# Kernel optimization log

Measured on AMD Instinct MI355X. Metric: run time of the kernel, lower is better.

Reference implementation:

```python
import jax, jax.numpy as jnp
import numpy as np

HEADS = 12
EPS_RMS = 1e-6
EPS_LN = 1e-5


def _rms_inorm(x, w):
    # torch.std over spatial dims (unbiased, ddof=1); no mean subtraction
    std = jnp.std(x, axis=(2, 3), keepdims=True, ddof=1)
    return x / (std + EPS_RMS) * w[None, :, None, None]


def _layernorm(x, w, b):
    m = jnp.mean(x, axis=-1, keepdims=True)
    v = jnp.var(x, axis=-1, keepdims=True)
    return (x - m) / jnp.sqrt(v + EPS_LN) * w + b


def setup_inputs() -> dict:
    key = jax.random.key(0)
    ks = jax.random.split(key, 16)
    B, C, H, W = 8, 768, 64, 64
    hd = C // HEADS
    s = 0.02
    return {
        "x": jax.random.normal(ks[0], (B, C, H, W), jnp.float32),
        "bcs": jnp.zeros((1, 2), jnp.int32),
        "norm1_w": jnp.ones((C,), jnp.float32),
        "norm2_w": jnp.ones((C,), jnp.float32),
        "mlpn_w": jnp.ones((C,), jnp.float32),
        "Win": jax.random.normal(ks[1], (3 * C, C), jnp.float32) * s,
        "bin_": jnp.zeros((3 * C,), jnp.float32),
        "Wout": jax.random.normal(ks[2], (C, C), jnp.float32) * s,
        "bout": jnp.zeros((C,), jnp.float32),
        "qn_w": jnp.ones((hd,), jnp.float32),
        "qn_b": jnp.zeros((hd,), jnp.float32),
        "kn_w": jnp.ones((hd,), jnp.float32),
        "kn_b": jnp.zeros((hd,), jnp.float32),
        "gamma_att": jnp.full((C,), 1e-6, jnp.float32),
        "gamma_mlp": jnp.full((C,), 1e-6, jnp.float32),
        "W1": jax.random.normal(ks[3], (C, 4 * C), jnp.float32) * s,
        "b1": jnp.zeros((4 * C,), jnp.float32),
        "W2": jax.random.normal(ks[4], (4 * C, C), jnp.float32) * s,
        "b2": jnp.zeros((C,), jnp.float32),
    }


def reference(x, bcs, norm1_w, norm2_w, mlpn_w, Win, bin_, Wout, bout,
              qn_w, qn_b, kn_w, kn_b, gamma_att, gamma_mlp, W1, b1, W2, b2):
    B, C, H, W = x.shape
    hd = C // HEADS
    scale = 1.0 / jnp.sqrt(jnp.asarray(hd, x.dtype))

    h = _rms_inorm(x, norm1_w)
    # 1x1 conv QKV: [B, 3C, H, W]
    qkv = jnp.einsum('bchw,oc->bohw', h, Win) + bin_[None, :, None, None]
    # b (he c3) h w -> b he h w c3, then split into q,k,v of head_dim each
    qkv = qkv.reshape(B, HEADS, 3 * hd, H, W).transpose(0, 1, 3, 4, 2)
    q, k, v = jnp.split(qkv, 3, axis=-1)  # each [B, he, H, W, hd]
    q = _layernorm(q, qn_w, qn_b)
    k = _layernorm(k, kn_w, kn_b)

    # row attention: attend along W for each row h
    sx = jnp.einsum('bnhqc,bnhkc->bnhqk', q, k) * scale
    xx = jnp.einsum('bnhqk,bnhkc->bnhqc', jax.nn.softmax(sx, axis=-1), v)
    # column attention: attend along H for each column w
    sy = jnp.einsum('bnqwc,bnkwc->bnwqk', q, k) * scale
    xy = jnp.einsum('bnwqk,bnkwc->bnqwc', jax.nn.softmax(sy, axis=-1), v)

    a = (xx + xy) * 0.5  # [B, he, H, W, hd]
    a = a.transpose(0, 1, 4, 2, 3).reshape(B, C, H, W)
    a = _rms_inorm(a, norm2_w)
    a = jnp.einsum('bchw,oc->bohw', a, Wout) + bout[None, :, None, None]
    x1 = a * gamma_att[None, :, None, None] + x

    t = x1.transpose(0, 2, 3, 1)  # [B, H, W, C]
    m = jax.nn.gelu(t @ W1 + b1, approximate=False) @ W2 + b2
    m = m.transpose(0, 3, 1, 2)
    m = _rms_inorm(m, mlpn_w)
    return x1 + gamma_mlp[None, :, None, None] * m
```

## Files before the change

kernel.cpp:

```cpp
#include <hip/hip_runtime.h>

typedef __attribute__((ext_vector_type(8))) short short8;
typedef __attribute__((ext_vector_type(4))) float f32x4;
typedef __attribute__((ext_vector_type(4))) unsigned short u16x4;
typedef __attribute__((ext_vector_type(8))) unsigned short u16x8;

#define BDIM 8
#define CDIM 768
#define C3 2304
#define C4 3072
#define HEADS 12
#define HD 64
#define HWD 4096
#define TOKS 32768

__device__ __forceinline__ float bf2f(unsigned short u) {
    union { unsigned int i; float f; } x; x.i = ((unsigned int)u) << 16; return x.f;
}
__device__ __forceinline__ unsigned short f2bf(float f) {
    union { float f; unsigned int i; } x; x.f = f;
    unsigned int r = x.i + 0x7FFFu + ((x.i >> 16) & 1u);
    return (unsigned short)(r >> 16);
}

__device__ __forceinline__ void gload_lds16(const unsigned short* g, unsigned short* l) {
    __builtin_amdgcn_global_load_lds(
        (const __attribute__((address_space(1))) void*)g,
        (__attribute__((address_space(3))) void*)l, 16, 0, 0);
}

__global__ __launch_bounds__(256) void convert_f32_bf16(
    const float* __restrict__ src, unsigned short* __restrict__ dst, int n)
{
    int i = (blockIdx.x * 256 + threadIdx.x) * 4;
    if (i + 3 >= n + 4) return;
    if (i + 3 < n) {
        float4 v = *(const float4*)&src[i];
        dst[i + 0] = f2bf(v.x); dst[i + 1] = f2bf(v.y);
        dst[i + 2] = f2bf(v.z); dst[i + 3] = f2bf(v.w);
    }
}

__global__ __launch_bounds__(256) void transpose_w(
    const float* __restrict__ src, unsigned short* __restrict__ dst, int R, int Cc)
{
    const int n0 = blockIdx.x * 64, k0 = blockIdx.y * 64;
    __shared__ float t[64][65];
    #pragma unroll
    for (int s = 0; s < 16; ++s) {
        int flat = threadIdx.x + 256 * s;
        int i = flat >> 6, j = flat & 63;
        t[i][j] = src[(long)(k0 + i) * Cc + n0 + j];
    }
    __syncthreads();
    #pragma unroll
    for (int s = 0; s < 16; ++s) {
        int flat = threadIdx.x + 256 * s;
        int jn = flat >> 6, ik = flat & 63;
        dst[(long)(n0 + jn) * R + k0 + ik] = f2bf(t[ik][jn]);
    }
}

__global__ __launch_bounds__(256) void stats_spatial_f32(
    const float* __restrict__ x, const float* __restrict__ wgt,
    float* __restrict__ sout, float eps)
{
    const int bc = blockIdx.x;
    const int c = bc % CDIM;
    const float4* p4 = (const float4*)(x + (long)bc * HWD);
    float s = 0.f, ss = 0.f;
    #pragma unroll
    for (int k = 0; k < 4; ++k) {
        float4 v = p4[threadIdx.x + 256 * k];
        s  += v.x + v.y + v.z + v.w;
        ss += v.x * v.x + v.y * v.y + v.z * v.z + v.w * v.w;
    }
    #pragma unroll
    for (int m = 1; m < 64; m <<= 1) { s += __shfl_xor(s, m); ss += __shfl_xor(ss, m); }
    __shared__ float rs[4], rss[4];
    int w = threadIdx.x >> 6, lane = threadIdx.x & 63;
    if (lane == 0) { rs[w] = s; rss[w] = ss; }
    __syncthreads();
    if (threadIdx.x == 0) {
        float S = rs[0] + rs[1] + rs[2] + rs[3];
        float Q = rss[0] + rss[1] + rss[2] + rss[3];
        float var = (Q - S * S * (1.f / 4096.f)) * (1.f / 4095.f);
        sout[bc] = wgt[c] / (sqrtf(var) + eps);
    }
}

__global__ __launch_bounds__(256) void stats_spatial_bf16(
    const unsigned short* __restrict__ t, const float* __restrict__ wgt,
    float* __restrict__ sout, float eps)
{
    const int b = blockIdx.x / 12, cg = blockIdx.x % 12;
    const int sub = threadIdx.x & 15, tr = threadIdx.x >> 4;
    const unsigned short* base = t + (long)b * HWD * CDIM + cg * 64 + sub * 4;
    float s[4] = {0.f, 0.f, 0.f, 0.f}, q[4] = {0.f, 0.f, 0.f, 0.f};
    for (int i = 0; i < 256; ++i) {
        const int token = tr + 16 * i;
        u16x4 v = *(const u16x4*)(base + (long)token * CDIM);
        #pragma unroll
        for (int j = 0; j < 4; ++j) { float f = bf2f(v[j]); s[j] += f; q[j] += f * f; }
    }
    __shared__ float ssum[16][64], ssq[16][64];
    #pragma unroll
    for (int j = 0; j < 4; ++j) { ssum[tr][sub * 4 + j] = s[j]; ssq[tr][sub * 4 + j] = q[j]; }
    __syncthreads();
    if (threadIdx.x < 64) {
        const int c = threadIdx.x;
        float S = 0.f, Q = 0.f;
        #pragma unroll
        for (int r = 0; r < 16; ++r) { S += ssum[r][c]; Q += ssq[r][c]; }
        const float var = (Q - S * S * (1.f / 4096.f)) * (1.f / 4095.f);
        const int cglob = cg * 64 + c;
        sout[b * CDIM + cglob] = wgt[cglob] / (sqrtf(var) + eps);
    }
}

__global__ __launch_bounds__(256) void make_h(
    const float* __restrict__ x, const float* __restrict__ s1,
    unsigned short* __restrict__ h)
{
    const int hw0 = blockIdx.x * 64, c0 = blockIdx.y * 64, b = blockIdx.z;
    __shared__ float t[64][65];
    #pragma unroll
    for (int s = 0; s < 16; ++s) {
        int flat = threadIdx.x + 256 * s;
        int ci = flat >> 6, hj = flat & 63;
        t[ci][hj] = x[(long)(b * CDIM + c0 + ci) * HWD + hw0 + hj];
    }
    __syncthreads();
    #pragma unroll
    for (int s = 0; s < 16; ++s) {
        int flat = threadIdx.x + 256 * s;
        int hi = flat >> 6, cj = flat & 63;
        float v = t[cj][hi] * s1[b * CDIM + c0 + cj];
        h[(long)(b * HWD + hw0 + hi) * CDIM + c0 + cj] = f2bf(v);
    }
}

template<int GELU>
__global__ __launch_bounds__(512, 4) void gemm256(
    const unsigned short* __restrict__ A, const unsigned short* __restrict__ BT,
    const float* __restrict__ bias, unsigned short* __restrict__ out,
    int M, int N, int K)
{
    extern __shared__ unsigned short smem[];
    const int tid = threadIdx.x;
    const int lane = tid & 63, w = tid >> 6;
    const int wm = w >> 1, wn = w & 1;
    const int lr = lane & 15, g = lane >> 4;

    const int nwg = gridDim.x;
    const int logical = (blockIdx.x & 7) * (nwg >> 3) + (blockIdx.x >> 3);
    const int gnx = N >> 7;
    const int n0 = (logical % gnx) << 7;
    const int m0 = (logical / gnx) << 8;

    const int ka = (((tid & 3) ^ ((tid >> 3) & 3)) << 3);
    const unsigned short* aS0 = A + (long)(m0 + (tid >> 2)) * K + ka;
    const unsigned short* aS1 = A + (long)(m0 + 128 + (tid >> 2)) * K + ka;
    const unsigned short* bS = BT + (long)(n0 + (tid >> 2)) * K + ka;
    unsigned short* dA0 = smem + (tid & ~63) * 8;
    unsigned short* dA1 = dA0 + 4096;
    unsigned short* dB  = smem + 16384 + (tid & ~63) * 8;

#define GSTAGE(S) do { \
        gload_lds16(aS0, dA0 + (S) * 8192); \
        gload_lds16(aS1, dA1 + (S) * 8192); \
        gload_lds16(bS,  dB  + (S) * 4096); \
        aS0 += 32; aS1 += 32; bS += 32; } while (0)

    const int nsub = K >> 5;
    const int koff = ((g ^ ((lr >> 1) & 3)) << 3);
    const unsigned short* baseA = smem + (wm * 64 + lr) * 32 + koff;
    const unsigned short* baseB = smem + 16384 + (wn * 64 + lr) * 32 + koff;

    f32x4 acc[4][4] = {};

    GSTAGE(0); GSTAGE(1);

#define SUBTILE(U, STG, WAITN) do { \
        asm volatile("s_waitcnt vmcnt(" #WAITN ")" ::: "memory"); \
        __builtin_amdgcn_s_barrier(); \
        short8 bf[4], af[4]; \
        _Pragma("unroll") \
        for (int ni = 0; ni < 4; ++ni) bf[ni] = *(const short8*)(baseB + (U) * 4096 + ni * 512); \
        _Pragma("unroll") \
        for (int mi = 0; mi < 4; ++mi) af[mi] = *(const short8*)(baseA + (U) * 8192 + mi * 512); \
        asm volatile("s_waitcnt lgkmcnt(0)" ::: "memory"); \
        __builtin_amdgcn_s_barrier(); \
        __builtin_amdgcn_sched_barrier(0); \
        STG; \
        __builtin_amdgcn_s_setprio(1); \
        _Pragma("unroll") \
        for (int mi = 0; mi < 4; ++mi) \
            _Pragma("unroll") \
            for (int ni = 0; ni < 4; ++ni) \
                acc[mi][ni] = __builtin_amdgcn_mfma_f32_16x16x32_bf16(af[mi], bf[ni], acc[mi][ni], 0, 0, 0); \
        __builtin_amdgcn_s_setprio(0); \
        __builtin_amdgcn_sched_barrier(0); } while (0)

    for (int j2 = 0; j2 + 2 < nsub; j2 += 2) {
        SUBTILE(0, GSTAGE(0), 3);
        SUBTILE(1, GSTAGE(1), 3);
    }
    SUBTILE(0, , 3);
    SUBTILE(1, , 0);
#undef SUBTILE
#undef GSTAGE

    #pragma unroll
    for (int mi = 0; mi < 4; ++mi) {
        #pragma unroll
        for (int ni = 0; ni < 4; ++ni) {
            const int gcol = n0 + wn * 64 + ni * 16 + lr;
            const float bv = bias[gcol];
            #pragma unroll
            for (int r = 0; r < 4; ++r) {
                const int grow = m0 + wm * 64 + mi * 16 + g * 4 + r;
                float v = acc[mi][ni][r] + bv;
                if (GELU) v = 0.5f * v * (1.f + erff(v * 0.70710678118f));
                out[(long)grow * N + gcol] = f2bf(v);
            }
        }
    }
}

__global__ __launch_bounds__(256) void qk_layernorm(
    unsigned short* __restrict__ qkv,
    const float* __restrict__ qw, const float* __restrict__ qb,
    const float* __restrict__ kw, const float* __restrict__ kb)
{
    const int pairIdx = blockIdx.x * 16 + (threadIdx.x >> 4);
    const int token = pairIdx / HEADS, he = pairIdx % HEADS;
    const int c4 = (threadIdx.x & 15) * 4;
    const long base = (long)token * C3 + he * 192;
    #pragma unroll
    for (int which = 0; which < 2; ++which) {
        const long off = base + which * 64 + c4;
        u16x4 v = *(u16x4*)&qkv[off];
        float f[4];
        #pragma unroll
        for (int j = 0; j < 4; ++j) f[j] = bf2f(v[j]);
        float s = f[0] + f[1] + f[2] + f[3];
        float q = f[0] * f[0] + f[1] * f[1] + f[2] * f[2] + f[3] * f[3];
        #pragma unroll
        for (int m = 1; m < 16; m <<= 1) { s += __shfl_xor(s, m); q += __shfl_xor(q, m); }
        const float mean = s * (1.f / 64.f);
        const float var = q * (1.f / 64.f) - mean * mean;
        const float rstd = rsqrtf(var + 1e-5f);
        const float* W = which ? kw : qw;
        const float* Bv = which ? kb : qb;
        u16x4 o;
        #pragma unroll
        for (int j = 0; j < 4; ++j)
            o[j] = f2bf((f[j] - mean) * rstd * W[c4 + j] + Bv[c4 + j]);
        *(u16x4*)&qkv[off] = o;
    }
}

template<int AXIS>
__global__ __launch_bounds__(128) void attn_axial(
    const unsigned short* __restrict__ qkv, unsigned short* __restrict__ a)
{
    __shared__ unsigned short lds[2][2][64 * 72];
    const int tid = threadIdx.x;
    const int lane = tid & 63, w = tid >> 6;
    const int lineG = blockIdx.x * 2 + w;
    const int b = lineG / 768;
    const int rem = lineG - b * 768;
    const int he = rem >> 6, line = rem & 63;
    const int ts = (AXIS == 0) ? 1 : 64;
    const long token0 = (long)b * HWD + (AXIS == 0 ? line * 64 : line);
    const long qbase = token0 * C3 + he * 192;
    unsigned short* VT = &lds[w][0][0];
    unsigned short* P  = &lds[w][1][0];
    const int lr = lane & 15, g = lane >> 4;

    {
        const int keyr = lane >> 3, d8 = (lane & 7) << 3;
        #pragma unroll
        for (int it = 0; it < 8; ++it) {
            const int key = it * 8 + keyr;
            u16x8 v = *(const u16x8*)&qkv[qbase + (long)key * ts * C3 + 128 + d8];
            #pragma unroll
            for (int j = 0; j < 8; ++j) VT[(d8 + j) * 72 + key] = v[j];
        }
    }

    short8 qf[4][2], kf[4][2];
    #pragma unroll
    for (int i = 0; i < 4; ++i)
        #pragma unroll
        for (int kk = 0; kk < 2; ++kk) {
            const long rb = qbase + (long)(i * 16 + lr) * ts * C3 + kk * 32 + g * 8;
            qf[i][kk] = *(const short8*)&qkv[rb];
            kf[i][kk] = *(const short8*)&qkv[rb + 64];
        }

    f32x4 acc[4][4] = {};
    #pragma unroll
    for (int mi = 0; mi < 4; ++mi)
        #pragma unroll
        for (int ni = 0; ni < 4; ++ni) {
            acc[mi][ni] = __builtin_amdgcn_mfma_f32_16x16x32_bf16(qf[mi][0], kf[ni][0], acc[mi][ni], 0, 0, 0);
            acc[mi][ni] = __builtin_amdgcn_mfma_f32_16x16x32_bf16(qf[mi][1], kf[ni][1], acc[mi][ni], 0, 0, 0);
        }

    #pragma unroll
    for (int mi = 0; mi < 4; ++mi)
        #pragma unroll
        for (int r = 0; r < 4; ++r) {
            float mx = -1e30f;
            #pragma unroll
            for (int ni = 0; ni < 4; ++ni) {
                float v = acc[mi][ni][r] * 0.125f; acc[mi][ni][r] = v; mx = fmaxf(mx, v);
            }
            #pragma unroll
            for (int m = 1; m < 16; m <<= 1) mx = fmaxf(mx, __shfl_xor(mx, m));
            float s = 0.f;
            #pragma unroll
            for (int ni = 0; ni < 4; ++ni) {
                float e = __expf(acc[mi][ni][r] - mx); acc[mi][ni][r] = e; s += e;
            }
            #pragma unroll
            for (int m = 1; m < 16; m <<= 1) s += __shfl_xor(s, m);
            const float inv = 1.f / s;
            const int row = mi * 16 + 4 * g + r;
            #pragma unroll
            for (int ni = 0; ni < 4; ++ni)
                P[row * 72 + ni * 16 + lr] = f2bf(acc[mi][ni][r] * inv);
        }
    __syncthreads();

    short8 pa[4][2], vb[4][2];
    #pragma unroll
    for (int i = 0; i < 4; ++i)
        #pragma unroll
        for (int kk = 0; kk < 2; ++kk) {
            pa[i][kk] = *(const short8*)&P[(i * 16 + lr) * 72 + kk * 32 + g * 8];
            vb[i][kk] = *(const short8*)&VT[(i * 16 + lr) * 72 + kk * 32 + g * 8];
        }
    f32x4 o2[4][4] = {};
    #pragma unroll
    for (int mi = 0; mi < 4; ++mi)
        #pragma unroll
        for (int ni = 0; ni < 4; ++ni) {
            o2[mi][ni] = __builtin_amdgcn_mfma_f32_16x16x32_bf16(pa[mi][0], vb[ni][0], o2[mi][ni], 0, 0, 0);
            o2[mi][ni] = __builtin_amdgcn_mfma_f32_16x16x32_bf16(pa[mi][1], vb[ni][1], o2[mi][ni], 0, 0, 0);
        }

    #pragma unroll
    for (int mi = 0; mi < 4; ++mi)
        #pragma unroll
        for (int r = 0; r < 4; ++r) {
            const int q = mi * 16 + 4 * g + r;
            const long tok = token0 + (long)q * ts;
            #pragma unroll
            for (int ni = 0; ni < 4; ++ni) {
                const int d = ni * 16 + lr;
                const long addr = tok * CDIM + he * 64 + d;
                const float v = o2[mi][ni][r] * 0.5f;
                if (AXIS == 0) a[addr] = f2bf(v);
                else           a[addr] = f2bf(bf2f(a[addr]) + v);
            }
        }
}

__global__ __launch_bounds__(256) void scale_inplace(
    unsigned short* __restrict__ a, const float* __restrict__ s2)
{
    const long i = ((long)blockIdx.x * 256 + threadIdx.x) * 4;
    const int c = (int)(i % CDIM);
    const int b = (int)(i / ((long)CDIM * HWD));
    u16x4 v = *(u16x4*)&a[i];
    u16x4 o;
    #pragma unroll
    for (int j = 0; j < 4; ++j) o[j] = f2bf(bf2f(v[j]) * s2[b * CDIM + c + j]);
    *(u16x4*)&a[i] = o;
}

__global__ __launch_bounds__(256) void x1_combine(
    const unsigned short* __restrict__ o, const float* __restrict__ x,
    const float* __restrict__ gamma, float* __restrict__ dout,
    unsigned short* __restrict__ x1b)
{
    const int hw0 = blockIdx.x * 64, c0 = blockIdx.y * 64, b = blockIdx.z;
    __shared__ float t[64][65];
    #pragma unroll
    for (int s = 0; s < 16; ++s) {
        int flat = threadIdx.x + 256 * s;
        int i = flat >> 6, j = flat & 63;
        t[i][j] = bf2f(o[(long)(b * HWD + hw0 + i) * CDIM + c0 + j]);
    }
    __syncthreads();
    #pragma unroll
    for (int s = 0; s < 16; ++s) {
        int flat = threadIdx.x + 256 * s;
        int j = flat >> 6, i = flat & 63;
        const long xi = (long)(b * CDIM + c0 + j) * HWD + hw0 + i;
        float v = x[xi] + gamma[c0 + j] * t[i][j];
        dout[xi] = v;
        t[i][j] = v;
    }
    __syncthreads();
    #pragma unroll
    for (int s = 0; s < 16; ++s) {
        int flat = threadIdx.x + 256 * s;
        int i = flat >> 6, j = flat & 63;
        x1b[(long)(b * HWD + hw0 + i) * CDIM + c0 + j] = f2bf(t[i][j]);
    }
}

__global__ __launch_bounds__(256) void final_combine(
    const unsigned short* __restrict__ m, const float* __restrict__ gm,
    const float* __restrict__ s3, float* __restrict__ dout)
{
    const int hw0 = blockIdx.x * 64, c0 = blockIdx.y * 64, b = blockIdx.z;
    __shared__ float t[64][65];
    #pragma unroll
    for (int s = 0; s < 16; ++s) {
        int flat = threadIdx.x + 256 * s;
        int i = flat >> 6, j = flat & 63;
        t[i][j] = bf2f(m[(long)(b * HWD + hw0 + i) * CDIM + c0 + j]);
    }
    __syncthreads();
    #pragma unroll
    for (int s = 0; s < 16; ++s) {
        int flat = threadIdx.x + 256 * s;
        int j = flat >> 6, i = flat & 63;
        const long xi = (long)(b * CDIM + c0 + j) * HWD + hw0 + i;
        dout[xi] = dout[xi] + gm[c0 + j] * s3[b * CDIM + c0 + j] * t[i][j];
    }
}

extern "C" void kernel_launch(void* const* d_in, const int* in_sizes, int n_in,
                              void* d_out, int out_size, void* d_ws, size_t ws_size,
                              hipStream_t stream) {
    const float* x      = (const float*)d_in[0];
    const float* n1w    = (const float*)d_in[2];
    const float* n2w    = (const float*)d_in[3];
    const float* mlw    = (const float*)d_in[4];
    const float* Win    = (const float*)d_in[5];
    const float* bin    = (const float*)d_in[6];
    const float* Wout   = (const float*)d_in[7];
    const float* bout   = (const float*)d_in[8];
    const float* qn_w   = (const float*)d_in[9];
    const float* qn_b   = (const float*)d_in[10];
    const float* kn_w   = (const float*)d_in[11];
    const float* kn_b   = (const float*)d_in[12];
    const float* gatt   = (const float*)d_in[13];
    const float* gmlp   = (const float*)d_in[14];
    const float* W1     = (const float*)d_in[15];
    const float* b1     = (const float*)d_in[16];
    const float* W2     = (const float*)d_in[17];
    const float* b2     = (const float*)d_in[18];
    float* dout = (float*)d_out;
    char* ws = (char*)d_ws;

    unsigned short* wQ  = (unsigned short*)(ws);
    unsigned short* wO  = (unsigned short*)(ws + (4L << 20));
    unsigned short* w1t = (unsigned short*)(ws + (6L << 20));
    unsigned short* w2t = (unsigned short*)(ws + (11L << 20));
    float* s1 = (float*)(ws + (16L << 20));
    float* s2 = s1 + 6144;
    float* s3 = s2 + 6144;
    unsigned short* bufH = (unsigned short*)(ws + (17L << 20));
    unsigned short* bufQ = (unsigned short*)(ws + (65L << 20));
    unsigned short* bufA = (unsigned short*)(ws + (209L << 20));

    convert_f32_bf16<<<1728, 256, 0, stream>>>(Win, wQ, C3 * CDIM);
    convert_f32_bf16<<<576, 256, 0, stream>>>(Wout, wO, CDIM * CDIM);
    transpose_w<<<dim3(C4 / 64, CDIM / 64), 256, 0, stream>>>(W1, w1t, CDIM, C4);
    transpose_w<<<dim3(CDIM / 64, C4 / 64), 256, 0, stream>>>(W2, w2t, C4, CDIM);

    stats_spatial_f32<<<BDIM * CDIM, 256, 0, stream>>>(x, n1w, s1, 1e-6f);
    make_h<<<dim3(64, 12, 8), 256, 0, stream>>>(x, s1, bufH);

    gemm256<0><<<(TOKS / 256) * (C3 / 128), 512, 49152, stream>>>(bufH, wQ, bin, bufQ, TOKS, C3, CDIM);
    qk_layernorm<<<TOKS * HEADS / 16, 256, 0, stream>>>(bufQ, qn_w, qn_b, kn_w, kn_b);

    attn_axial<0><<<BDIM * HEADS * 64 / 2, 128, 0, stream>>>(bufQ, bufA);
    attn_axial<1><<<BDIM * HEADS * 64 / 2, 128, 0, stream>>>(bufQ, bufA);

    stats_spatial_bf16<<<BDIM * 12, 256, 0, stream>>>(bufA, n2w, s2, 1e-6f);
    scale_inplace<<<TOKS * CDIM / 1024, 256, 0, stream>>>(bufA, s2);
    gemm256<0><<<(TOKS / 256) * (CDIM / 128), 512, 49152, stream>>>(bufA, wO, bout, bufH, TOKS, CDIM, CDIM);
    x1_combine<<<dim3(64, 12, 8), 256, 0, stream>>>(bufH, x, gatt, dout, bufA);

    for (int ch = 0; ch < 2; ++ch) {
        const unsigned short* x1c = bufA + (long)ch * 16384 * CDIM;
        unsigned short* mc = bufH + (long)ch * 16384 * CDIM;
        gemm256<1><<<(16384 / 256) * (C4 / 128), 512, 49152, stream>>>(x1c, w1t, b1, bufQ, 16384, C4, CDIM);
        gemm256<0><<<(16384 / 256) * (CDIM / 128), 512, 49152, stream>>>(bufQ, w2t, b2, mc, 16384, CDIM, C4);
    }

    stats_spatial_bf16<<<BDIM * 12, 256, 0, stream>>>(bufH, mlw, s3, 1e-6f);
    final_combine<<<dim3(64, 12, 8), 256, 0, stream>>>(bufH, gmlp, s3, dout);
}
```

Measured before the change: 923.1 us.

## Fuse QK layernorm into axial attention and drop fp32 x1 round-trip

Removes the standalone qk_layernorm pass. Each axial attention kernel now normalizes its Q and K fragments in registers as it loads them, using cross-lane shuffles, so the in-place read and write of the Q/K part of the qkv buffer goes away. The cost is doing the layernorm twice, once per axis. Separately, x1_combine no longer writes fp32 x1 into the output. final_combine rebuilds the result from the bf16 x1 copy plus the scaled MLP branch, which cuts fp32 traffic but adds bf16 rounding to the residual term.

```diff
diff --git a/kernel.cpp b/kernel.cpp
--- a/kernel.cpp
+++ b/kernel.cpp
@@ -228,42 +228,12 @@
     }
 }
 
-__global__ __launch_bounds__(256) void qk_layernorm(
-    unsigned short* __restrict__ qkv,
-    const float* __restrict__ qw, const float* __restrict__ qb,
-    const float* __restrict__ kw, const float* __restrict__ kb)
-{
-    const int pairIdx = blockIdx.x * 16 + (threadIdx.x >> 4);
-    const int token = pairIdx / HEADS, he = pairIdx % HEADS;
-    const int c4 = (threadIdx.x & 15) * 4;
-    const long base = (long)token * C3 + he * 192;
-    #pragma unroll
-    for (int which = 0; which < 2; ++which) {
-        const long off = base + which * 64 + c4;
-        u16x4 v = *(u16x4*)&qkv[off];
-        float f[4];
-        #pragma unroll
-        for (int j = 0; j < 4; ++j) f[j] = bf2f(v[j]);
-        float s = f[0] + f[1] + f[2] + f[3];
-        float q = f[0] * f[0] + f[1] * f[1] + f[2] * f[2] + f[3] * f[3];
-        #pragma unroll
-        for (int m = 1; m < 16; m <<= 1) { s += __shfl_xor(s, m); q += __shfl_xor(q, m); }
-        const float mean = s * (1.f / 64.f);
-        const float var = q * (1.f / 64.f) - mean * mean;
-        const float rstd = rsqrtf(var + 1e-5f);
-        const float* W = which ? kw : qw;
-        const float* Bv = which ? kb : qb;
-        u16x4 o;
-        #pragma unroll
-        for (int j = 0; j < 4; ++j)
-            o[j] = f2bf((f[j] - mean) * rstd * W[c4 + j] + Bv[c4 + j]);
-        *(u16x4*)&qkv[off] = o;
-    }
-}
-
 template<int AXIS>
 __global__ __launch_bounds__(128) void attn_axial(
-    const unsigned short* __restrict__ qkv, unsigned short* __restrict__ a)
+    const unsigned short* __restrict__ qkv,
+    const float* __restrict__ qn_w, const float* __restrict__ qn_b,
+    const float* __restrict__ kn_w, const float* __restrict__ kn_b,
+    unsigned short* __restrict__ a)
 {
     __shared__ unsigned short lds[2][2][64 * 72];
     const int tid = threadIdx.x;
@@ -292,13 +262,40 @@
 
     short8 qf[4][2], kf[4][2];
     #pragma unroll
-    for (int i = 0; i < 4; ++i)
-        #pragma unroll
-        for (int kk = 0; kk < 2; ++kk) {
-            const long rb = qbase + (long)(i * 16 + lr) * ts * C3 + kk * 32 + g * 8;
-            qf[i][kk] = *(const short8*)&qkv[rb];
-            kf[i][kk] = *(const short8*)&qkv[rb + 64];
-        }
+    for (int i = 0; i < 4; ++i) {
+        const long rb = qbase + (long)(i * 16 + lr) * ts * C3 + g * 8;
+        u16x8 qv0 = *(const u16x8*)&qkv[rb];
+        u16x8 qv1 = *(const u16x8*)&qkv[rb + 32];
+        u16x8 kv0 = *(const u16x8*)&qkv[rb + 64];
+        u16x8 kv1 = *(const u16x8*)&qkv[rb + 96];
+        float q0[8], q1[8], k0[8], k1[8];
+        float qs = 0.f, qq = 0.f, ks = 0.f, kq = 0.f;
+        #pragma unroll
+        for (int j = 0; j < 8; ++j) {
+            q0[j] = bf2f(qv0[j]); q1[j] = bf2f(qv1[j]);
+            k0[j] = bf2f(kv0[j]); k1[j] = bf2f(kv1[j]);
+            qs += q0[j] + q1[j]; qq += q0[j] * q0[j] + q1[j] * q1[j];
+            ks += k0[j] + k1[j]; kq += k0[j] * k0[j] + k1[j] * k1[j];
+        }
+        qs += __shfl_xor(qs, 16); qs += __shfl_xor(qs, 32);
+        qq += __shfl_xor(qq, 16); qq += __shfl_xor(qq, 32);
+        ks += __shfl_xor(ks, 16); ks += __shfl_xor(ks, 32);
+        kq += __shfl_xor(kq, 16); kq += __shfl_xor(kq, 32);
+        const float qm = qs * (1.f / 64.f);
+        const float qr = rsqrtf(qq * (1.f / 64.f) - qm * qm + 1e-5f);
+        const float km = ks * (1.f / 64.f);
+        const float kr = rsqrtf(kq * (1.f / 64.f) - km * km + 1e-5f);
+        short8 oq0, oq1, ok0, ok1;
+        #pragma unroll
+        for (int j = 0; j < 8; ++j) {
+            const int c0 = g * 8 + j, c1 = 32 + g * 8 + j;
+            oq0[j] = (short)f2bf((q0[j] - qm) * qr * qn_w[c0] + qn_b[c0]);
+            oq1[j] = (short)f2bf((q1[j] - qm) * qr * qn_w[c1] + qn_b[c1]);
+            ok0[j] = (short)f2bf((k0[j] - km) * kr * kn_w[c0] + kn_b[c0]);
+            ok1[j] = (short)f2bf((k1[j] - km) * kr * kn_w[c1] + kn_b[c1]);
+        }
+        qf[i][0] = oq0; qf[i][1] = oq1; kf[i][0] = ok0; kf[i][1] = ok1;
+    }
 
     f32x4 acc[4][4] = {};
     #pragma unroll
@@ -384,8 +381,7 @@
 
 __global__ __launch_bounds__(256) void x1_combine(
     const unsigned short* __restrict__ o, const float* __restrict__ x,
-    const float* __restrict__ gamma, float* __restrict__ dout,
-    unsigned short* __restrict__ x1b)
+    const float* __restrict__ gamma, unsigned short* __restrict__ x1b)
 {
     const int hw0 = blockIdx.x * 64, c0 = blockIdx.y * 64, b = blockIdx.z;
     __shared__ float t[64][65];
@@ -401,9 +397,7 @@
         int flat = threadIdx.x + 256 * s;
         int j = flat >> 6, i = flat & 63;
         const long xi = (long)(b * CDIM + c0 + j) * HWD + hw0 + i;
-        float v = x[xi] + gamma[c0 + j] * t[i][j];
-        dout[xi] = v;
-        t[i][j] = v;
+        t[i][j] = x[xi] + gamma[c0 + j] * t[i][j];
     }
     __syncthreads();
     #pragma unroll
@@ -415,8 +409,9 @@
 }
 
 __global__ __launch_bounds__(256) void final_combine(
-    const unsigned short* __restrict__ m, const float* __restrict__ gm,
-    const float* __restrict__ s3, float* __restrict__ dout)
+    const unsigned short* __restrict__ x1b, const unsigned short* __restrict__ m,
+    const float* __restrict__ gm, const float* __restrict__ s3,
+    float* __restrict__ dout)
 {
     const int hw0 = blockIdx.x * 64, c0 = blockIdx.y * 64, b = blockIdx.z;
     __shared__ float t[64][65];
@@ -424,15 +419,15 @@
     for (int s = 0; s < 16; ++s) {
         int flat = threadIdx.x + 256 * s;
         int i = flat >> 6, j = flat & 63;
-        t[i][j] = bf2f(m[(long)(b * HWD + hw0 + i) * CDIM + c0 + j]);
+        const long tok = (long)(b * HWD + hw0 + i) * CDIM + c0 + j;
+        t[i][j] = bf2f(x1b[tok]) + gm[c0 + j] * s3[b * CDIM + c0 + j] * bf2f(m[tok]);
     }
     __syncthreads();
     #pragma unroll
     for (int s = 0; s < 16; ++s) {
         int flat = threadIdx.x + 256 * s;
         int j = flat >> 6, i = flat & 63;
-        const long xi = (long)(b * CDIM + c0 + j) * HWD + hw0 + i;
-        dout[xi] = dout[xi] + gm[c0 + j] * s3[b * CDIM + c0 + j] * t[i][j];
+        dout[(long)(b * CDIM + c0 + j) * HWD + hw0 + i] = t[i][j];
     }
 }
 
@@ -480,15 +475,14 @@
     make_h<<<dim3(64, 12, 8), 256, 0, stream>>>(x, s1, bufH);
 
     gemm256<0><<<(TOKS / 256) * (C3 / 128), 512, 49152, stream>>>(bufH, wQ, bin, bufQ, TOKS, C3, CDIM);
-    qk_layernorm<<<TOKS * HEADS / 16, 256, 0, stream>>>(bufQ, qn_w, qn_b, kn_w, kn_b);
-
-    attn_axial<0><<<BDIM * HEADS * 64 / 2, 128, 0, stream>>>(bufQ, bufA);
-    attn_axial<1><<<BDIM * HEADS * 64 / 2, 128, 0, stream>>>(bufQ, bufA);
+
+    attn_axial<0><<<BDIM * HEADS * 64 / 2, 128, 0, stream>>>(bufQ, qn_w, qn_b, kn_w, kn_b, bufA);
+    attn_axial<1><<<BDIM * HEADS * 64 / 2, 128, 0, stream>>>(bufQ, qn_w, qn_b, kn_w, kn_b, bufA);
 
     stats_spatial_bf16<<<BDIM * 12, 256, 0, stream>>>(bufA, n2w, s2, 1e-6f);
     scale_inplace<<<TOKS * CDIM / 1024, 256, 0, stream>>>(bufA, s2);
     gemm256<0><<<(TOKS / 256) * (CDIM / 128), 512, 49152, stream>>>(bufA, wO, bout, bufH, TOKS, CDIM, CDIM);
-    x1_combine<<<dim3(64, 12, 8), 256, 0, stream>>>(bufH, x, gatt, dout, bufA);
+    x1_combine<<<dim3(64, 12, 8), 256, 0, stream>>>(bufH, x, gatt, bufA);
 
     for (int ch = 0; ch < 2; ++ch) {
         const unsigned short* x1c = bufA + (long)ch * 16384 * CDIM;
@@ -498,5 +492,5 @@
     }
 
     stats_spatial_bf16<<<BDIM * 12, 256, 0, stream>>>(bufH, mlw, s3, 1e-6f);
-    final_combine<<<dim3(64, 12, 8), 256, 0, stream>>>(bufH, gmlp, s3, dout);
-}
+    final_combine<<<dim3(64, 12, 8), 256, 0, stream>>>(bufA, bufH, gmlp, s3, dout);
+}
```

New measurement: 957.4 us. +3.7%, slower.
